# Optimization experiments

Measured on AMD Instinct MI355X. Metric: run time of the kernel, lower is better.

The kernel has to match this reference:

```python
import jax, jax.numpy as jnp
import numpy as np

N = 200000   # num_nodes
D = 64       # embedding_dims
B = 4096     # batch of target nodes (batched per-edge processing)
K = 128      # padded in-neighbor count per target
W = 20       # window_size (history deque length)
H = 128      # hidden_size


def setup_inputs() -> dict:
    key = jax.random.key(0)
    ks = jax.random.split(key, 14)
    return {
        "adj_time": jax.random.uniform(ks[0], (N,), jnp.float32),          # last-seen times in [0,1)
        "gc": jax.random.uniform(ks[1], (N,), jnp.float32),                 # per-node centrality scalar (dict_gc)
        "cur_time": jnp.ones((1,), jnp.float32),                            # current event time (>= all stored times)
        "neigh_mask": jnp.ones((B, K), jnp.float32),                        # 1 = valid neighbor slot
        "hist_feat": jax.random.normal(ks[2], (B, W, 2 * D), jnp.float32),  # feature_dict[...]['feature'] deque
        "hist_time": jax.random.uniform(ks[3], (B, W), jnp.float32),        # feature_dict[...]['time'] deque
        "t2v_w": jax.random.normal(ks[4], (D,), jnp.float32),               # Time2Vec('cos') weights
        "t2v_b": jax.random.normal(ks[5], (D,), jnp.float32),
        "node_w": jax.random.normal(ks[6], (D,), jnp.float32),              # linear_node: Linear(1, D)
        "node_b": jax.random.normal(ks[7], (D,), jnp.float32),
        "att_w": jax.random.normal(ks[8], (2 * D,), jnp.float32),           # Attention: score = cat(a,b) @ w + b
        "att_b": jax.random.normal(ks[9], (1,), jnp.float32),
        "weight": jax.random.normal(ks[10], (H, 4 * D), jnp.float32) * 0.05,
        "targets": jax.random.randint(ks[11], (B,), 0, N),
        "neigh_idx": jax.random.randint(ks[12], (B, K), 0, N),
    }


def reference(adj_time, gc, cur_time, neigh_mask, hist_feat, hist_time,
              t2v_w, t2v_b, node_w, node_b, att_w, att_b, weight,
              targets, neigh_idx):
    t = cur_time[0]

    def node_encoding(idx):
        # Time2Vec('cos'): first channel linear, rest cos(w*dt+b)
        dt = jnp.abs(t - adj_time[idx])[..., None]            # [..., 1]
        phase = t2v_w * dt + t2v_b                            # [..., D]
        tv = jnp.concatenate([phase[..., :1], jnp.cos(phase[..., 1:])], axis=-1)
        feat = jax.nn.relu(tv + gc[idx][..., None] * node_w + node_b)
        # F.normalize (L2 over feature dim)
        return feat / jnp.maximum(jnp.linalg.norm(feat, axis=-1, keepdims=True), 1e-12)

    tgt_feat = node_encoding(targets)       # [B, D]
    ngh_feat = node_encoding(neigh_idx)     # [B, K, D]

    # Decayer(2, 'log'): time_score = 1 / (2 * log(e + dt))
    time_score = 1.0 / (2.0 * jnp.log(jnp.e + (t - adj_time[neigh_idx])))   # [B, K]
    # Attention score between target and each neighbor encoding
    att = (tgt_feat @ att_w[:D])[:, None] \
        + jnp.einsum("bkd,d->bk", ngh_feat, att_w[D:]) + att_b[0]           # [B, K]
    score = jax.nn.leaky_relu(time_score + att, 0.01) * neigh_mask          # [B, K]
    neigh_agg = jnp.einsum("bk,bkd->bd", score, ngh_feat)                   # [B, D]

    combined = jnp.concatenate([tgt_feat, neigh_agg], axis=-1)              # [B, 2D]

    # History aggregation with Decayer(2, 'rev'): w = 1 / (2 * (1 + dt))
    hist_w = 1.0 / (2.0 * (1.0 + (t - hist_time)))                          # [B, W]
    hist_agg = jnp.einsum("bw,bwd->bd", hist_w, hist_feat)                  # [B, 2D]

    feat4 = jnp.concatenate([hist_agg, combined], axis=-1)                  # [B, 4D]
    return jax.nn.relu(feat4 @ weight.T)                                    # [B, H]
```

## Files before the change

### kernel.cpp

```cpp
#include <hip/hip_runtime.h>
#include <math.h>

#define NN 200000
#define DD 64
#define BB 4096
#define KK 128
#define WW 20
#define HH 128
#define TPB 512
#define RPB 4

#define INV2PI 0.15915494309189535f

__device__ __forceinline__ float fast_rcp(float x) { return __builtin_amdgcn_rcpf(x); }
__device__ __forceinline__ float fast_rsq(float x) { return __builtin_amdgcn_rsqf(x); }

__global__ __launch_bounds__(512, 8) void fused(
    const float* __restrict__ adj_time, const float* __restrict__ gc,
    const float* __restrict__ cur_time, const float* __restrict__ neigh_mask,
    const float* __restrict__ hist_feat, const float* __restrict__ hist_time,
    const float* __restrict__ t2v_w, const float* __restrict__ t2v_b,
    const float* __restrict__ node_w, const float* __restrict__ node_b,
    const float* __restrict__ att_w, const float* __restrict__ att_b,
    const float* __restrict__ weight,
    const int* __restrict__ targets, const int* __restrict__ neigh_idx,
    float* __restrict__ out)
{
    const int b0   = blockIdx.x * RPB;
    const int tid  = threadIdx.x;
    const int lane = tid & 63;
    const int wv   = tid >> 6;

    __shared__ float4 dtg[RPB * KK];
    __shared__ float  hws[RPB][WW];
    __shared__ float  stL[RPB];
    __shared__ float  p3p[RPB][DD];
    __shared__ float  tile[RPB * 256];
    __shared__ float  wl[128 * 33];

    const float t = cur_time[0];

    const int   slot = tid;
    const int   idx  = neigh_idx[b0 * KK + slot];
    const float m    = neigh_mask[b0 * KK + slot];
    const float at   = adj_time[idx];
    const float g    = gc[idx];
    const float dt   = fabsf(t - at);
    const float ts   = fast_rcp(2.0f * __logf(2.71828182845904523536f + (t - at)));
    dtg[slot] = make_float4(dt, g, 0.f, 0.f);

    if (tid >= 256 && tid < 256 + RPB * WW) {
        int i = tid - 256;
        int r = i / WW, w = i - r * WW;
        hws[r][w] = fast_rcp(2.0f * (1.0f + (t - hist_time[(b0 + r) * WW + w])));
    }

    if (wv < RPB) {
        int   tg  = targets[b0 + wv];
        float dtT = fabsf(t - adj_time[tg]);
        float gT  = gc[tg];
        float ph  = fmaf(t2v_w[lane], dtT, t2v_b[lane]);
        float tv_ = (lane == 0) ? ph : __cosf(ph);
        float f   = fmaxf(tv_ + fmaf(gT, node_w[lane], node_b[lane]), 0.f);
        float ss  = f * f;
#pragma unroll
        for (int off = 32; off; off >>= 1) ss += __shfl_xor(ss, off, 64);
        float invn = fast_rsq(fmaxf(ss, 1e-24f));
        float tfn  = f * invn;
        float sdt  = tfn * att_w[lane];
#pragma unroll
        for (int off = 32; off; off >>= 1) sdt += __shfl_xor(sdt, off, 64);
        if (lane == 0) stL[wv] = sdt;
        tile[wv * 256 + 128 + lane] = tfn;
    }
    __syncthreads();

    {
        const int   r  = slot >> 7;
        const float ab = att_b[0];
        float s2, sd;
        {
            float ph = fmaf(t2v_w[0], dt, t2v_b[0]);
            float f  = fmaxf(ph + fmaf(g, node_w[0], node_b[0]), 0.f);
            s2 = f * f;
            sd = f * att_w[64];
        }
#pragma unroll 4
        for (int d = 1; d < 64; ++d) {
            float ph = fmaf(t2v_w[d], dt, t2v_b[d]);
            float f  = fmaxf(__cosf(ph) + fmaf(g, node_w[d], node_b[d]), 0.f);
            s2 = fmaf(f, f, s2);
            sd = fmaf(f, att_w[64 + d], sd);
        }
        float invn = fast_rsq(fmaxf(s2, 1e-24f));
        float sc   = ts + stL[r] + sd * invn + ab;
        sc = (sc > 0.f) ? sc : 0.01f * sc;
        dtg[slot].z = sc * m * invn;
    }

    if (tid < 128) {
        int r  = tid >> 5;
        int c4 = tid & 31;
        const float4* hf = (const float4*)(hist_feat + (size_t)(b0 + r) * WW * 128) + c4;
        float4 s4 = make_float4(0.f, 0.f, 0.f, 0.f);
#pragma unroll 4
        for (int w = 0; w < WW; ++w) {
            float  hw = hws[r][w];
            float4 v  = hf[w * 32];
            s4.x = fmaf(hw, v.x, s4.x);
            s4.y = fmaf(hw, v.y, s4.y);
            s4.z = fmaf(hw, v.z, s4.z);
            s4.w = fmaf(hw, v.w, s4.w);
        }
        *(float4*)(tile + r * 256 + c4 * 4) = s4;
    }
    __syncthreads();

    const int r3   = wv >> 1;
    const int half = wv & 1;
    float acc3 = 0.f;
    {
        float sc  = (lane == 0) ? 1.f : INV2PI;
        float pw  = t2v_w[lane] * sc;
        float pb  = t2v_b[lane] * sc;
        float nw  = node_w[lane];
        float nb2 = node_b[lane];
        const int base = r3 * KK + half * 64;
#pragma unroll 4
        for (int k = 0; k < 64; ++k) {
            float4 dgw = dtg[base + k];
            float  ph  = fmaf(pw, dgw.x, pb);
            float  cv  = __builtin_amdgcn_cosf(ph);
            float  tv_ = lane ? cv : ph;
            float  f   = fmaxf(tv_ + fmaf(dgw.y, nw, nb2), 0.f);
            acc3 = fmaf(dgw.z, f, acc3);
        }
    }
    if (half) p3p[r3][lane] = acc3;
    __syncthreads();
    if (!half) tile[r3 * 256 + 192 + lane] = acc3 + p3p[r3][lane];

    const int h  = tid & 127;
    const int gg = tid >> 7;
    const float* tb = tile + gg * 256;
    float acc = 0.f;

    for (int c = 0; c < 8; ++c) {
        __syncthreads();
#pragma unroll
        for (int i = 0; i < 8; ++i) {
            int l  = i * TPB + tid;
            int hh = l >> 5, jj = l & 31;
            wl[hh * 33 + jj] = weight[hh * 256 + c * 32 + jj];
        }
        __syncthreads();

#pragma unroll
        for (int jj = 0; jj < 32; jj += 4) {
            float w0 = wl[h * 33 + jj + 0];
            float w1 = wl[h * 33 + jj + 1];
            float w2 = wl[h * 33 + jj + 2];
            float w3 = wl[h * 33 + jj + 3];
            float4 f0 = *(const float4*)(tb + c * 32 + jj);
            acc += w0 * f0.x + w1 * f0.y + w2 * f0.z + w3 * f0.w;
        }
    }

    out[(size_t)(b0 + gg) * 128 + h] = fmaxf(acc, 0.f);
}

extern "C" void kernel_launch(void* const* d_in, const int* in_sizes, int n_in,
                              void* d_out, int out_size, void* d_ws, size_t ws_size,
                              hipStream_t stream) {
    const float* adj_time  = (const float*)d_in[0];
    const float* gc        = (const float*)d_in[1];
    const float* cur_time  = (const float*)d_in[2];
    const float* neigh_mask= (const float*)d_in[3];
    const float* hist_feat = (const float*)d_in[4];
    const float* hist_time = (const float*)d_in[5];
    const float* t2v_w     = (const float*)d_in[6];
    const float* t2v_b     = (const float*)d_in[7];
    const float* node_w    = (const float*)d_in[8];
    const float* node_b    = (const float*)d_in[9];
    const float* att_w     = (const float*)d_in[10];
    const float* att_b     = (const float*)d_in[11];
    const float* weight    = (const float*)d_in[12];
    const int*   targets   = (const int*)d_in[13];
    const int*   neigh_idx = (const int*)d_in[14];

    float* out = (float*)d_out;

    fused<<<BB / RPB, TPB, 0, stream>>>(adj_time, gc, cur_time, neigh_mask,
                                        hist_feat, hist_time, t2v_w, t2v_b,
                                        node_w, node_b, att_w, att_b, weight,
                                        targets, neigh_idx, out);
}
```

Before: 138.2 us.

## Broadcast neighbor params via readlane and restructure final GEMV with swizzled float4 weights

The neighbor-aggregation loop now loads each wave's 64 neighbor (dt, gc, score) values once per lane and broadcasts them with readlane, instead of reading shared memory on every iteration. The loop is fully unrolled. The output projection stores weight tiles as XOR-swizzled float4 to avoid LDS bank conflicts. Each thread now covers one hidden unit across all 4 rows for an 8-column slice, and the four partial sums are reduced through shared memory. This cuts LDS traffic and load instruction count, at the cost of an extra reduction step, more barriers, and higher register pressure from the unroll.

```diff
diff --git a/kernel.cpp b/kernel.cpp
--- a/kernel.cpp
+++ b/kernel.cpp
@@ -14,6 +14,9 @@
 
 __device__ __forceinline__ float fast_rcp(float x) { return __builtin_amdgcn_rcpf(x); }
 __device__ __forceinline__ float fast_rsq(float x) { return __builtin_amdgcn_rsqf(x); }
+__device__ __forceinline__ float rlane(float v, int l) {
+    return __int_as_float(__builtin_amdgcn_readlane(__float_as_int(v), l));
+}
 
 __global__ __launch_bounds__(512, 8) void fused(
     const float* __restrict__ adj_time, const float* __restrict__ gc,
@@ -36,7 +39,7 @@
     __shared__ float  stL[RPB];
     __shared__ float  p3p[RPB][DD];
     __shared__ float  tile[RPB * 256];
-    __shared__ float  wl[128 * 33];
+    __shared__ float4 wl4[128 * 8];
 
     const float t = cur_time[0];
 
@@ -118,22 +121,24 @@
 
     const int r3   = wv >> 1;
     const int half = wv & 1;
+    float4 myk = dtg[r3 * KK + half * 64 + lane];
     float acc3 = 0.f;
     {
-        float sc  = (lane == 0) ? 1.f : INV2PI;
-        float pw  = t2v_w[lane] * sc;
-        float pb  = t2v_b[lane] * sc;
+        float scn = (lane == 0) ? 1.f : INV2PI;
+        float pw  = t2v_w[lane] * scn;
+        float pb  = t2v_b[lane] * scn;
         float nw  = node_w[lane];
         float nb2 = node_b[lane];
-        const int base = r3 * KK + half * 64;
-#pragma unroll 4
+#pragma unroll
         for (int k = 0; k < 64; ++k) {
-            float4 dgw = dtg[base + k];
-            float  ph  = fmaf(pw, dgw.x, pb);
-            float  cv  = __builtin_amdgcn_cosf(ph);
-            float  tv_ = lane ? cv : ph;
-            float  f   = fmaxf(tv_ + fmaf(dgw.y, nw, nb2), 0.f);
-            acc3 = fmaf(dgw.z, f, acc3);
+            float kdt = rlane(myk.x, k);
+            float kg  = rlane(myk.y, k);
+            float kw  = rlane(myk.z, k);
+            float ph  = fmaf(pw, kdt, pb);
+            float cv  = __builtin_amdgcn_cosf(ph);
+            float tv_ = lane ? cv : ph;
+            float f   = fmaxf(tv_ + fmaf(kg, nw, nb2), 0.f);
+            acc3 = fmaf(kw, f, acc3);
         }
     }
     if (half) p3p[r3][lane] = acc3;
@@ -141,32 +146,45 @@
     if (!half) tile[r3 * 256 + 192 + lane] = acc3 + p3p[r3][lane];
 
     const int h  = tid & 127;
-    const int gg = tid >> 7;
-    const float* tb = tile + gg * 256;
-    float acc = 0.f;
+    const int sq = tid >> 7;
+    const int hx = h & 7;
+    const float4* w4g = (const float4*)weight;
+    float accr[4] = {0.f, 0.f, 0.f, 0.f};
 
     for (int c = 0; c < 8; ++c) {
         __syncthreads();
 #pragma unroll
-        for (int i = 0; i < 8; ++i) {
+        for (int i = 0; i < 2; ++i) {
             int l  = i * TPB + tid;
-            int hh = l >> 5, jj = l & 31;
-            wl[hh * 33 + jj] = weight[hh * 256 + c * 32 + jj];
+            int hh = l >> 3, gg = l & 7;
+            wl4[hh * 8 + (gg ^ (hh & 7))] = w4g[hh * 64 + c * 8 + gg];
         }
         __syncthreads();
 
-#pragma unroll
-        for (int jj = 0; jj < 32; jj += 4) {
-            float w0 = wl[h * 33 + jj + 0];
-            float w1 = wl[h * 33 + jj + 1];
-            float w2 = wl[h * 33 + jj + 2];
-            float w3 = wl[h * 33 + jj + 3];
-            float4 f0 = *(const float4*)(tb + c * 32 + jj);
-            acc += w0 * f0.x + w1 * f0.y + w2 * f0.z + w3 * f0.w;
-        }
-    }
-
-    out[(size_t)(b0 + gg) * 128 + h] = fmaxf(acc, 0.f);
+        float4 wa = wl4[h * 8 + ((sq * 2)     ^ hx)];
+        float4 wb = wl4[h * 8 + ((sq * 2 + 1) ^ hx)];
+        const int jb = c * 32 + sq * 8;
+#pragma unroll
+        for (int r = 0; r < 4; ++r) {
+            float4 f0 = *(const float4*)(tile + r * 256 + jb);
+            float4 f1 = *(const float4*)(tile + r * 256 + jb + 4);
+            accr[r] += wa.x * f0.x + wa.y * f0.y + wa.z * f0.z + wa.w * f0.w
+                     + wb.x * f1.x + wb.y * f1.y + wb.z * f1.z + wb.w * f1.w;
+        }
+    }
+
+    __syncthreads();
+    float* prow = (float*)dtg;
+#pragma unroll
+    for (int r = 0; r < 4; ++r)
+        prow[(r * 4 + sq) * 128 + h] = accr[r];
+    __syncthreads();
+    {
+        const int r2 = tid >> 7;
+        float s = prow[(r2 * 4 + 0) * 128 + h] + prow[(r2 * 4 + 1) * 128 + h]
+                + prow[(r2 * 4 + 2) * 128 + h] + prow[(r2 * 4 + 3) * 128 + h];
+        out[(size_t)(b0 + r2) * 128 + h] = fmaxf(s, 0.f);
+    }
 }
 
 extern "C" void kernel_launch(void* const* d_in, const int* in_sizes, int n_in,
```

After: 135.8 us. About the same (-1.8%).

## Read weight directly per thread with split-K and overlap history aggregation earlier

Applied to the files above, without the earlier changes.

The final GEMV no longer stages weight through shared memory in eight chunks with paired barriers. Each thread now reads float4 rows of weight straight from global/L2, computes a quarter of the K dimension for all four rows, and reduces the partials through shared memory reused from dtg. The history aggregation, including the per-window decay weights, moves to the upper threads at the start so it overlaps the neighbor-encoding pass, and one barrier is removed. This cuts barriers and LDS footprint, which may raise occupancy. In exchange it relies on uncoalesced per-thread weight loads, since each thread reads a separate 256-byte row segment.

```diff
diff --git a/kernel.cpp b/kernel.cpp
--- a/kernel.cpp
+++ b/kernel.cpp
@@ -32,11 +32,9 @@
     const int wv   = tid >> 6;
 
     __shared__ float4 dtg[RPB * KK];
-    __shared__ float  hws[RPB][WW];
     __shared__ float  stL[RPB];
     __shared__ float  p3p[RPB][DD];
     __shared__ float  tile[RPB * 256];
-    __shared__ float  wl[128 * 33];
 
     const float t = cur_time[0];
 
@@ -49,10 +47,22 @@
     const float ts   = fast_rcp(2.0f * __logf(2.71828182845904523536f + (t - at)));
     dtg[slot] = make_float4(dt, g, 0.f, 0.f);
 
-    if (tid >= 256 && tid < 256 + RPB * WW) {
-        int i = tid - 256;
-        int r = i / WW, w = i - r * WW;
-        hws[r][w] = fast_rcp(2.0f * (1.0f + (t - hist_time[(b0 + r) * WW + w])));
+    if (tid >= 384) {
+        const int r  = (tid >> 5) & 3;
+        const int c4 = tid & 31;
+        const float*  ht = hist_time + (size_t)(b0 + r) * WW;
+        const float4* hf = (const float4*)(hist_feat + (size_t)(b0 + r) * WW * 128) + c4;
+        float4 s4 = make_float4(0.f, 0.f, 0.f, 0.f);
+#pragma unroll 4
+        for (int w = 0; w < WW; ++w) {
+            float  hw = fast_rcp(2.0f * (1.0f + (t - ht[w])));
+            float4 v  = hf[w * 32];
+            s4.x = fmaf(hw, v.x, s4.x);
+            s4.y = fmaf(hw, v.y, s4.y);
+            s4.z = fmaf(hw, v.z, s4.z);
+            s4.w = fmaf(hw, v.w, s4.w);
+        }
+        *(float4*)(tile + r * 256 + c4 * 4) = s4;
     }
 
     if (wv < RPB) {
@@ -73,12 +83,9 @@
         if (lane == 0) stL[wv] = sdt;
         tile[wv * 256 + 128 + lane] = tfn;
     }
-    __syncthreads();
 
+    float s2, sd;
     {
-        const int   r  = slot >> 7;
-        const float ab = att_b[0];
-        float s2, sd;
         {
             float ph = fmaf(t2v_w[0], dt, t2v_b[0]);
             float f  = fmaxf(ph + fmaf(g, node_w[0], node_b[0]), 0.f);
@@ -92,27 +99,14 @@
             s2 = fmaf(f, f, s2);
             sd = fmaf(f, att_w[64 + d], sd);
         }
+    }
+    __syncthreads();
+
+    {
         float invn = fast_rsq(fmaxf(s2, 1e-24f));
-        float sc   = ts + stL[r] + sd * invn + ab;
+        float sc   = ts + stL[slot >> 7] + sd * invn + att_b[0];
         sc = (sc > 0.f) ? sc : 0.01f * sc;
         dtg[slot].z = sc * m * invn;
-    }
-
-    if (tid < 128) {
-        int r  = tid >> 5;
-        int c4 = tid & 31;
-        const float4* hf = (const float4*)(hist_feat + (size_t)(b0 + r) * WW * 128) + c4;
-        float4 s4 = make_float4(0.f, 0.f, 0.f, 0.f);
-#pragma unroll 4
-        for (int w = 0; w < WW; ++w) {
-            float  hw = hws[r][w];
-            float4 v  = hf[w * 32];
-            s4.x = fmaf(hw, v.x, s4.x);
-            s4.y = fmaf(hw, v.y, s4.y);
-            s4.z = fmaf(hw, v.z, s4.z);
-            s4.w = fmaf(hw, v.w, s4.w);
-        }
-        *(float4*)(tile + r * 256 + c4 * 4) = s4;
     }
     __syncthreads();
 
@@ -120,9 +114,9 @@
     const int half = wv & 1;
     float acc3 = 0.f;
     {
-        float sc  = (lane == 0) ? 1.f : INV2PI;
-        float pw  = t2v_w[lane] * sc;
-        float pb  = t2v_b[lane] * sc;
+        float scn = (lane == 0) ? 1.f : INV2PI;
+        float pw  = t2v_w[lane] * scn;
+        float pb  = t2v_b[lane] * scn;
         float nw  = node_w[lane];
         float nb2 = node_b[lane];
         const int base = r3 * KK + half * 64;
@@ -139,34 +133,39 @@
     if (half) p3p[r3][lane] = acc3;
     __syncthreads();
     if (!half) tile[r3 * 256 + 192 + lane] = acc3 + p3p[r3][lane];
+    __syncthreads();
 
     const int h  = tid & 127;
-    const int gg = tid >> 7;
-    const float* tb = tile + gg * 256;
-    float acc = 0.f;
-
-    for (int c = 0; c < 8; ++c) {
-        __syncthreads();
-#pragma unroll
-        for (int i = 0; i < 8; ++i) {
-            int l  = i * TPB + tid;
-            int hh = l >> 5, jj = l & 31;
-            wl[hh * 33 + jj] = weight[hh * 256 + c * 32 + jj];
-        }
-        __syncthreads();
-
-#pragma unroll
-        for (int jj = 0; jj < 32; jj += 4) {
-            float w0 = wl[h * 33 + jj + 0];
-            float w1 = wl[h * 33 + jj + 1];
-            float w2 = wl[h * 33 + jj + 2];
-            float w3 = wl[h * 33 + jj + 3];
-            float4 f0 = *(const float4*)(tb + c * 32 + jj);
-            acc += w0 * f0.x + w1 * f0.y + w2 * f0.z + w3 * f0.w;
-        }
+    const int sq = tid >> 7;
+    const float4* w4 = (const float4*)weight + h * 64 + sq * 16;
+    const int jb = sq * 64;
+    float a0 = 0.f, a1 = 0.f, a2 = 0.f, a3 = 0.f;
+#pragma unroll 4
+    for (int j4 = 0; j4 < 16; ++j4) {
+        float4 w  = w4[j4];
+        const int jo = jb + j4 * 4;
+        float4 f0 = *(const float4*)(tile + 0 * 256 + jo);
+        float4 f1 = *(const float4*)(tile + 1 * 256 + jo);
+        float4 f2 = *(const float4*)(tile + 2 * 256 + jo);
+        float4 f3 = *(const float4*)(tile + 3 * 256 + jo);
+        a0 += w.x * f0.x + w.y * f0.y + w.z * f0.z + w.w * f0.w;
+        a1 += w.x * f1.x + w.y * f1.y + w.z * f1.z + w.w * f1.w;
+        a2 += w.x * f2.x + w.y * f2.y + w.z * f2.z + w.w * f2.w;
+        a3 += w.x * f3.x + w.y * f3.y + w.z * f3.z + w.w * f3.w;
     }
 
-    out[(size_t)(b0 + gg) * 128 + h] = fmaxf(acc, 0.f);
+    float* prow = (float*)dtg;
+    prow[(0 * 4 + sq) * 128 + h] = a0;
+    prow[(1 * 4 + sq) * 128 + h] = a1;
+    prow[(2 * 4 + sq) * 128 + h] = a2;
+    prow[(3 * 4 + sq) * 128 + h] = a3;
+    __syncthreads();
+    {
+        const int r2 = tid >> 7;
+        float s = prow[(r2 * 4 + 0) * 128 + h] + prow[(r2 * 4 + 1) * 128 + h]
+                + prow[(r2 * 4 + 2) * 128 + h] + prow[(r2 * 4 + 3) * 128 + h];
+        out[(size_t)(b0 + r2) * 128 + h] = fmaxf(s, 0.f);
+    }
 }
 
 extern "C" void kernel_launch(void* const* d_in, const int* in_sizes, int n_in,
```

Result: faster. 133.9 us (-3.1%).
